# Performance work log

Hardware: AMD Instinct MI355X
Metric: run time of the kernel (lower is better)

Reference implementation:

```python
import math
import jax, jax.numpy as jnp
import numpy as np

L, H, K, NH, V, DFF = 6, 512, 512, 8, 64, 1024
B, T, S = 8, 512, 512
PAD = 0


def _ln(x, g, b, eps=1e-5):
    m = jnp.mean(x, -1, keepdims=True)
    v = jnp.mean((x - m) ** 2, -1, keepdims=True)
    return (x - m) * jax.lax.rsqrt(v + eps) * g + b


def _mha(Q, Kin, Vin, mask, wq, bq, wk, bk, wv, bv, wo, bo, g, b):
    # weights stored [in, out]
    B_, Tq, Hd = Q.shape
    dk = wq.shape[1] // NH
    dv = wv.shape[1] // NH
    q = (Q @ wq + bq).reshape(B_, Tq, NH, dk).transpose(0, 2, 1, 3)
    k = (Kin @ wk + bk).reshape(B_, -1, NH, dk).transpose(0, 2, 1, 3)
    v = (Vin @ wv + bv).reshape(B_, -1, NH, dv).transpose(0, 2, 1, 3)
    scores = jnp.einsum('bhqd,bhkd->bhqk', q, k) / jnp.sqrt(jnp.float32(dk))
    scores = jnp.where(mask[:, None, :, :], jnp.float32(-1e9), scores)
    attn = jax.nn.softmax(scores, axis=-1)
    ctx = jnp.einsum('bhqk,bhkd->bhqd', attn, v).transpose(0, 2, 1, 3).reshape(B_, Tq, Hd)
    return _ln(ctx @ wo + bo + Q, g, b)


def _pe(t, d):
    pos = jnp.arange(t, dtype=jnp.float32)[:, None]
    div = jnp.exp(jnp.arange(0, d, 2, dtype=jnp.float32) * (-math.log(10000.0) / d))
    pe = jnp.zeros((t, d), jnp.float32)
    pe = pe.at[:, 0::2].set(jnp.sin(pos * div)).at[:, 1::2].set(jnp.cos(pos * div))
    return pe


def setup_inputs() -> dict:
    key = jax.random.key(0)
    ks = iter(jax.random.split(key, 40))
    nrm = lambda shape, s=0.02: jax.random.normal(next(ks), shape, jnp.float32) * s
    inp = {
        'smiles_index': jax.random.randint(next(ks), (B, T), 0, V, dtype=jnp.int32),
        'enc_outputs': jax.random.normal(next(ks), (B, S, H), jnp.float32),
        'enc_pad_mask': jnp.zeros((B, 1, S), bool),
        'tgt_len': T,
        'mol_emb': nrm((V, H), 1.0).at[PAD].set(0.0),  # padding_idx=0 row zeroed
        # self-attn stacks [L, ...]
        'sa_wq': nrm((L, H, K)), 'sa_bq': jnp.zeros((L, K)),
        'sa_wk': nrm((L, H, K)), 'sa_bk': jnp.zeros((L, K)),
        'sa_wv': nrm((L, H, H)), 'sa_bv': jnp.zeros((L, H)),
        'sa_wo': nrm((L, H, H)), 'sa_bo': jnp.zeros((L, H)),
        'ln1_g': jnp.ones((L, H)), 'ln1_b': jnp.zeros((L, H)),
        # cross-attn stacks
        'ea_wq': nrm((L, H, K)), 'ea_bq': jnp.zeros((L, K)),
        'ea_wk': nrm((L, H, K)), 'ea_bk': jnp.zeros((L, K)),
        'ea_wv': nrm((L, H, H)), 'ea_bv': jnp.zeros((L, H)),
        'ea_wo': nrm((L, H, H)), 'ea_bo': jnp.zeros((L, H)),
        'ln2_g': jnp.ones((L, H)), 'ln2_b': jnp.zeros((L, H)),
        # conv1x1 FFN == per-position linear
        'c1_w': nrm((L, H, DFF)), 'c1_b': jnp.zeros((L, DFF)),
        'c2_w': nrm((L, DFF, H)), 'c2_b': jnp.zeros((L, H)),
        'ln3_g': jnp.ones((L, H)), 'ln3_b': jnp.zeros((L, H)),
    }
    return inp


def reference(smiles_index, enc_outputs, enc_pad_mask, tgt_len, mol_emb,
              sa_wq, sa_bq, sa_wk, sa_bk, sa_wv, sa_bv, sa_wo, sa_bo, ln1_g, ln1_b,
              ea_wq, ea_bq, ea_wk, ea_bk, ea_wv, ea_bv, ea_wo, ea_bo, ln2_g, ln2_b,
              c1_w, c1_b, c2_w, c2_b, ln3_g, ln3_b):
    b, t = smiles_index.shape
    s = enc_outputs.shape[1]
    # embeddings + sinusoidal positional encoding (dropout is identity in eval)
    x = mol_emb[smiles_index] + _pe(t, mol_emb.shape[1])[None]
    # masks: pad (key == pad_id) OR causal upper-triangular
    pad = (smiles_index == PAD)[:, None, :]                 # [B,1,T] -> broadcast over queries
    causal = jnp.triu(jnp.ones((t, t), bool), 1)[None]      # [1,T,T]
    self_mask = pad | causal                                # [B,T,T]
    enc_mask = jnp.broadcast_to(enc_pad_mask, (b, t, s))    # [B,T,S]
    for l in range(L):
        x = _mha(x, x, x, self_mask,
                 sa_wq[l], sa_bq[l], sa_wk[l], sa_bk[l], sa_wv[l], sa_bv[l],
                 sa_wo[l], sa_bo[l], ln1_g[l], ln1_b[l])
        x = _mha(x, enc_outputs, enc_outputs, enc_mask,
                 ea_wq[l], ea_bq[l], ea_wk[l], ea_bk[l], ea_wv[l], ea_bv[l],
                 ea_wo[l], ea_bo[l], ln2_g[l], ln2_b[l])
        h = jax.nn.relu(x @ c1_w[l] + c1_b[l])
        y = h @ c2_w[l] + c2_b[l]
        x = _ln(y + x, ln3_g[l], ln3_b[l])
    return x
```

## Files before the change

### kernel.cpp

```cpp
#include <hip/hip_runtime.h>
#include <hip/hip_bf16.h>
#include <math.h>

#define NL   6
#define HD   512
#define NHD  8
#define DK   64
#define DFFN 1024
#define NB   8
#define TT   512
#define MROWS (NB*TT)

typedef __hip_bfloat16 bf16;
typedef __attribute__((ext_vector_type(8))) short short8v;
typedef __attribute__((ext_vector_type(4))) float f32x4;

__device__ __forceinline__ float wave_sum(float v) {
#pragma unroll
  for (int off = 32; off; off >>= 1) v += __shfl_xor(v, off);
  return v;
}
__device__ __forceinline__ unsigned short f2bf(float x) {
  __hip_bfloat16 h = __float2bfloat16(x);
  return *reinterpret_cast<unsigned short*>(&h);
}

__device__ __forceinline__ void gload16(const void* g, void* l) {
  __builtin_amdgcn_global_load_lds(
      (const __attribute__((address_space(1))) unsigned int*)g,
      (__attribute__((address_space(3))) unsigned int*)l, 16, 0, 0);
}

__global__ __launch_bounds__(256)
void wprep_kernel(const float* __restrict__ W, bf16* __restrict__ Wt, int Kd, int Nd,
                  int dstRowOff, int dstSlabRows) {
  __shared__ float t[32][33];
  const size_t src = (size_t)blockIdx.z * Kd * Nd;
  const size_t dst = (size_t)blockIdx.z * dstSlabRows * Kd;
  const int n0 = blockIdx.x * 32, k0 = blockIdx.y * 32;
  const int tx = threadIdx.x & 31, ty = threadIdx.x >> 5;
#pragma unroll
  for (int j = 0; j < 4; ++j)
    t[ty + j * 8][tx] = W[src + (size_t)(k0 + ty + j * 8) * Nd + n0 + tx];
  __syncthreads();
#pragma unroll
  for (int j = 0; j < 4; ++j)
    Wt[dst + (size_t)(dstRowOff + n0 + ty + j * 8) * Kd + k0 + tx] =
        __float2bfloat16(t[tx][ty + j * 8]);
}

__global__ __launch_bounds__(256)
void bcat_kernel(const float* __restrict__ b0, const float* __restrict__ b1,
                 const float* __restrict__ b2, float* __restrict__ out, int nseg) {
  const int l = blockIdx.x;
  const int stride = 512 * nseg;
  for (int i = threadIdx.x; i < stride; i += 256) {
    const int seg = i >> 9, off = i & 511;
    const float* src = seg == 0 ? b0 : (seg == 1 ? b1 : b2);
    out[(size_t)l * stride + i] = src[(size_t)l * 512 + off];
  }
}

__global__ __launch_bounds__(256)
void cvtbf16_kernel(const float* __restrict__ in, unsigned short* __restrict__ out) {
  const int i = (blockIdx.x * 256 + threadIdx.x) * 4;
  float4 v = *(const float4*)(in + i);
  out[i + 0] = f2bf(v.x); out[i + 1] = f2bf(v.y);
  out[i + 2] = f2bf(v.z); out[i + 3] = f2bf(v.w);
}

__global__ __launch_bounds__(256)
void embed_pe_kernel(const int* __restrict__ idx, const float* __restrict__ emb,
                     float* __restrict__ x, unsigned short* __restrict__ xb) {
  const int row = blockIdx.x;
  const int t = row & (TT - 1);
  const int tok = idx[row];
  const float cdiv = -0.017988946009466842f;
#pragma unroll
  for (int e0 = 0; e0 < 2; ++e0) {
    const int e = threadIdx.x + e0 * 256;
    const float div = __expf((float)(e & ~1) * cdiv);
    const float ang = (float)t * div;
    const float pe = (e & 1) ? cosf(ang) : sinf(ang);
    const float v = emb[(size_t)tok * HD + e] + pe;
    x[(size_t)row * HD + e] = v;
    xb[(size_t)row * HD + e] = f2bf(v);
  }
}

template<int TN, int OUT_BF16, int RELU>
__global__ __launch_bounds__(256)
void mgemm2_kernel(const bf16* __restrict__ A, const bf16* __restrict__ Bt,
                   const float* __restrict__ bias, float* __restrict__ Cf,
                   unsigned short* __restrict__ Cb, int M, int N, int K) {
  constexpr int NR = TN / 32;
  constexpr int BJ = TN / 32;
  __shared__ __attribute__((aligned(16))) char As[2][128 * 128];
  __shared__ __attribute__((aligned(16))) char Bs[2][TN * 128];

  const int tid = threadIdx.x, w = tid >> 6, lane = tid & 63;
  const int wm = w >> 1, wn = w & 1;
  const int m0 = blockIdx.x * 128, n0 = blockIdx.y * TN;
  const int lrow = lane >> 3;
  const int lchk = (lane & 7) ^ lrow;

  const bf16* ga[4];
#pragma unroll
  for (int j = 0; j < 4; ++j)
    ga[j] = A + (size_t)(m0 + w * 32 + j * 8 + lrow) * K + lchk * 8;
  const bf16* gb[BJ];
#pragma unroll
  for (int j = 0; j < BJ; ++j)
    gb[j] = Bt + (size_t)(n0 + w * (8 * BJ) + j * 8 + lrow) * K + lchk * 8;

  f32x4 acc[4][NR];
#pragma unroll
  for (int fm = 0; fm < 4; ++fm)
#pragma unroll
    for (int fn = 0; fn < NR; ++fn) acc[fm][fn] = (f32x4){0.f, 0.f, 0.f, 0.f};

  const int l4 = lane & 15;
  const int khb = (lane >> 4) * 16;

  auto issue = [&](int t, int buf) {
#pragma unroll
    for (int j = 0; j < 4; ++j)
      gload16(ga[j] + t * 64, &As[buf][(w * 32 + j * 8) * 128]);
#pragma unroll
    for (int j = 0; j < BJ; ++j)
      gload16(gb[j] + t * 64, &Bs[buf][(w * (8 * BJ) + j * 8) * 128]);
  };
  auto compute = [&](int buf) {
#pragma unroll
    for (int kk = 0; kk < 2; ++kk) {
      short8v af[4], bfv[NR];
#pragma unroll
      for (int fm = 0; fm < 4; ++fm) {
        const int r = wm * 64 + fm * 16 + l4;
        af[fm] = *(const short8v*)(&As[buf][r * 128 + ((kk * 64 + khb) ^ ((r & 7) << 4))]);
      }
#pragma unroll
      for (int fn = 0; fn < NR; ++fn) {
        const int r = wn * (TN / 2) + fn * 16 + l4;
        bfv[fn] = *(const short8v*)(&Bs[buf][r * 128 + ((kk * 64 + khb) ^ ((r & 7) << 4))]);
      }
#pragma unroll
      for (int fm = 0; fm < 4; ++fm)
#pragma unroll
        for (int fn = 0; fn < NR; ++fn)
          acc[fm][fn] = __builtin_amdgcn_mfma_f32_16x16x32_bf16(af[fm], bfv[fn], acc[fm][fn], 0, 0, 0);
    }
  };

  const int NT = K >> 6;
  issue(0, 0);
  for (int t = 0; t < NT; ++t) {
    __syncthreads();
    if (t + 1 < NT) issue(t + 1, (t + 1) & 1);
    compute(t & 1);
  }

  const int crow = (lane >> 4) * 4, ccol = l4;
#pragma unroll
  for (int fm = 0; fm < 4; ++fm)
#pragma unroll
    for (int fn = 0; fn < NR; ++fn) {
      const int gr = m0 + wm * 64 + fm * 16 + crow;
      const int gc = n0 + wn * (TN / 2) + fn * 16 + ccol;
      const float bs = bias[gc];
#pragma unroll
      for (int r = 0; r < 4; ++r) {
        float vv = acc[fm][fn][r] + bs;
        if (RELU) vv = fmaxf(vv, 0.f);
        if (OUT_BF16) Cb[(size_t)(gr + r) * N + gc] = f2bf(vv);
        else          Cf[(size_t)(gr + r) * N + gc] = vv;
      }
    }
}

template<int CAUSAL>
__global__ __launch_bounds__(256)
void mattn_kernel(const unsigned short* __restrict__ q, const unsigned short* __restrict__ kgl,
                  const unsigned short* __restrict__ vgl, unsigned short* __restrict__ ctx,
                  const int* __restrict__ idx, const unsigned char* __restrict__ emask,
                  int qstride, int kvstride) {
  __shared__ __attribute__((aligned(16))) unsigned short kt[64 * 64];
  __shared__ __attribute__((aligned(16))) unsigned short vt[64 * 64];
  __shared__ __attribute__((aligned(16))) unsigned short pl[4][16 * 64];
  __shared__ float km[64];

  const int bh = blockIdx.x;
  const int b = bh >> 3, h = bh & 7;
  const int qbase = blockIdx.y * 64;
  const int tid = threadIdx.x, w = tid >> 6, lane = tid & 63;
  const int l4 = lane & 15, g = lane >> 4;

  const unsigned short* qp = q + (size_t)(b * TT + qbase + w * 16 + l4) * qstride + h * DK + g * 8;
  short8v aq0 = *(const short8v*)qp;
  short8v aq1 = *(const short8v*)(qp + 32);

  float m_r[4], l_r[4];
  f32x4 acc_o[4];
#pragma unroll
  for (int r = 0; r < 4; ++r) { m_r[r] = -1e30f; l_r[r] = 0.f; }
#pragma unroll
  for (int f = 0; f < 4; ++f) acc_o[f] = (f32x4){0.f, 0.f, 0.f, 0.f};

  const int kvEnd = CAUSAL ? (qbase + 64) : TT;
  for (int kt0 = 0; kt0 < kvEnd; kt0 += 64) {
    __syncthreads();
    if (tid < 64) {
      const int kp = b * TT + kt0 + tid;
      const bool mk = CAUSAL ? (idx[kp] == 0) : (emask[kp] != 0);
      km[tid] = mk ? 1.f : 0.f;
    }
    {
      const int r = tid >> 2;
      const int bc = (tid & 3) * 32;
      const unsigned short* kp = kgl + (size_t)(b * TT + kt0 + r) * kvstride + h * DK + (bc >> 1);
      short8v ka = *(const short8v*)kp;
      short8v kb2 = *(const short8v*)(kp + 8);
      const int sw = (r & 7) << 4;
      *(short8v*)((char*)kt + r * 128 + (bc ^ sw)) = ka;
      *(short8v*)((char*)kt + r * 128 + ((bc + 16) ^ sw)) = kb2;
    }
    {
      const int k2 = (tid & 31) * 2;
      const int d0 = (tid >> 5) * 8;
      const unsigned short* vp0 = vgl + (size_t)(b * TT + kt0 + k2) * kvstride + h * DK + d0;
      const unsigned short* vp1 = vp0 + kvstride;
      short8v v0 = *(const short8v*)vp0;
      short8v v1 = *(const short8v*)vp1;
#pragma unroll
      for (int j = 0; j < 8; ++j) {
        const int d = d0 + j;
        const unsigned pk = ((unsigned)(unsigned short)v0[j]) | (((unsigned)(unsigned short)v1[j]) << 16);
        *(unsigned*)((char*)vt + d * 128 + ((k2 * 2) ^ ((d & 7) << 4))) = pk;
      }
    }
    __syncthreads();

    f32x4 s4[4];
#pragma unroll
    for (int f = 0; f < 4; ++f) {
      const int krow = f * 16 + l4;
      const int sw = (krow & 7) << 4;
      short8v bk0 = *(const short8v*)((const char*)kt + krow * 128 + ((g * 16) ^ sw));
      short8v bk1 = *(const short8v*)((const char*)kt + krow * 128 + ((64 + g * 16) ^ sw));
      f32x4 a = {};
      a = __builtin_amdgcn_mfma_f32_16x16x32_bf16(aq0, bk0, a, 0, 0, 0);
      a = __builtin_amdgcn_mfma_f32_16x16x32_bf16(aq1, bk1, a, 0, 0, 0);
      s4[f] = a;
    }

    float sc_r[4];
#pragma unroll
    for (int r = 0; r < 4; ++r) {
      const int qpos = qbase + w * 16 + g * 4 + r;
      float sf[4];
#pragma unroll
      for (int f = 0; f < 4; ++f) {
        const int kpos = kt0 + f * 16 + l4;
        float s = s4[f][r] * 0.125f;
        const bool msk = (km[f * 16 + l4] != 0.f) || (CAUSAL && kpos > qpos);
        sf[f] = msk ? -1e9f : s;
      }
      float mx = fmaxf(fmaxf(sf[0], sf[1]), fmaxf(sf[2], sf[3]));
#pragma unroll
      for (int off = 8; off; off >>= 1) mx = fmaxf(mx, __shfl_xor(mx, off));
      const float mn = fmaxf(m_r[r], mx);
      const float sc = __expf(m_r[r] - mn);
      m_r[r] = mn;
      sc_r[r] = sc;
      float ps = 0.f;
      const int prow = g * 4 + r;
      const int psw = (prow & 7) << 4;
#pragma unroll
      for (int f = 0; f < 4; ++f) {
        const float p = __expf(sf[f] - mn);
        ps += p;
        *(unsigned short*)((char*)pl[w] + prow * 128 + ((f * 32 + l4 * 2) ^ psw)) = f2bf(p);
      }
#pragma unroll
      for (int off = 8; off; off >>= 1) ps += __shfl_xor(ps, off);
      l_r[r] = l_r[r] * sc + ps;
    }

#pragma unroll
    for (int f = 0; f < 4; ++f)
#pragma unroll
      for (int r = 0; r < 4; ++r) acc_o[f][r] *= sc_r[r];

    const int asw = (l4 & 7) << 4;
    short8v pa0 = *(const short8v*)((const char*)pl[w] + l4 * 128 + ((g * 16) ^ asw));
    short8v pa1 = *(const short8v*)((const char*)pl[w] + l4 * 128 + ((g * 16 + 64) ^ asw));
#pragma unroll
    for (int f = 0; f < 4; ++f) {
      const int drow = f * 16 + l4;
      const int sw = (drow & 7) << 4;
      short8v vb0 = *(const short8v*)((const char*)vt + drow * 128 + ((g * 16) ^ sw));
      short8v vb1 = *(const short8v*)((const char*)vt + drow * 128 + ((g * 16 + 64) ^ sw));
      acc_o[f] = __builtin_amdgcn_mfma_f32_16x16x32_bf16(pa0, vb0, acc_o[f], 0, 0, 0);
      acc_o[f] = __builtin_amdgcn_mfma_f32_16x16x32_bf16(pa1, vb1, acc_o[f], 0, 0, 0);
    }
  }

  float rl[4];
#pragma unroll
  for (int r = 0; r < 4; ++r) rl[r] = 1.f / l_r[r];
#pragma unroll
  for (int f = 0; f < 4; ++f)
#pragma unroll
    for (int r = 0; r < 4; ++r) {
      const int row = qbase + w * 16 + g * 4 + r;
      const int col = h * DK + f * 16 + l4;
      ctx[(size_t)(b * TT + row) * HD + col] = f2bf(acc_o[f][r] * rl[r]);
    }
}

__global__ __launch_bounds__(256)
void ln_kernel(const float* __restrict__ y, const float* __restrict__ res,
               float* __restrict__ out, unsigned short* __restrict__ outb,
               const float* __restrict__ g, const float* __restrict__ bta) {
  const int row = blockIdx.x;
  const int tid = threadIdx.x;
  const int w = tid >> 6, lane = tid & 63;
  const float* yr = y + (size_t)row * HD;
  const float* rr = res + (size_t)row * HD;

  float v0 = yr[tid] + rr[tid];
  float v1 = yr[tid + 256] + rr[tid + 256];

  __shared__ float red[4];
  float s = wave_sum(v0 + v1);
  if (lane == 0) red[w] = s;
  __syncthreads();
  const float mean = (red[0] + red[1] + red[2] + red[3]) * (1.f / HD);
  __syncthreads();

  const float d0 = v0 - mean, d1 = v1 - mean;
  float qv = wave_sum(d0 * d0 + d1 * d1);
  if (lane == 0) red[w] = qv;
  __syncthreads();
  const float var = (red[0] + red[1] + red[2] + red[3]) * (1.f / HD);
  const float rstd = rsqrtf(var + 1e-5f);

  const float o0 = d0 * rstd * g[tid] + bta[tid];
  const float o1 = d1 * rstd * g[tid + 256] + bta[tid + 256];
  out[(size_t)row * HD + tid] = o0;
  out[(size_t)row * HD + tid + 256] = o1;
  outb[(size_t)row * HD + tid] = f2bf(o0);
  outb[(size_t)row * HD + tid + 256] = f2bf(o1);
}

extern "C" void kernel_launch(void* const* d_in, const int* in_sizes, int n_in,
                              void* d_out, int out_size, void* d_ws, size_t ws_size,
                              hipStream_t stream) {
  const int* idx = (const int*)d_in[0];
  const float* enc = (const float*)d_in[1];
  const unsigned char* emask = (const unsigned char*)d_in[2];
  const float* emb = (const float*)d_in[4];
  const float* sa_wq = (const float*)d_in[5];
  const float* sa_bq = (const float*)d_in[6];
  const float* sa_wk = (const float*)d_in[7];
  const float* sa_bk = (const float*)d_in[8];
  const float* sa_wv = (const float*)d_in[9];
  const float* sa_bv = (const float*)d_in[10];
  const float* sa_wo = (const float*)d_in[11];
  const float* sa_bo = (const float*)d_in[12];
  const float* ln1g = (const float*)d_in[13];
  const float* ln1b = (const float*)d_in[14];
  const float* ea_wq = (const float*)d_in[15];
  const float* ea_bq = (const float*)d_in[16];
  const float* ea_wk = (const float*)d_in[17];
  const float* ea_bk = (const float*)d_in[18];
  const float* ea_wv = (const float*)d_in[19];
  const float* ea_bv = (const float*)d_in[20];
  const float* ea_wo = (const float*)d_in[21];
  const float* ea_bo = (const float*)d_in[22];
  const float* ln2g = (const float*)d_in[23];
  const float* ln2b = (const float*)d_in[24];
  const float* c1w = (const float*)d_in[25];
  const float* c1b = (const float*)d_in[26];
  const float* c2w = (const float*)d_in[27];
  const float* c2b = (const float*)d_in[28];
  const float* ln3g = (const float*)d_in[29];
  const float* ln3b = (const float*)d_in[30];

  const size_t MH = (size_t)MROWS * HD;
  const size_t SQ = (size_t)HD * HD;
  char* ws = (char*)d_ws;
  float*          x    = (float*)(ws + 0);
  unsigned short* xb   = (unsigned short*)(ws + (8u << 20));
  unsigned short* qkvb = (unsigned short*)(ws + (12u << 20));
  unsigned short* qcb  = (unsigned short*)(ws + (24u << 20));
  unsigned short* kvb  = (unsigned short*)(ws + (28u << 20));
  unsigned short* cxb  = (unsigned short*)(ws + (36u << 20));
  float*          yb   = (float*)(ws + (40u << 20));
  unsigned short* encb = (unsigned short*)(ws + (48u << 20));
  bf16*           wt   = (bf16*)(ws + (52u << 20));
  float*          bcS  = (float*)(ws + (92u << 20));
  float*          bcKV = (float*)(ws + (93u << 20));
  unsigned short* hb   = qkvb;

  bf16* t_saqkv = wt;
  bf16* t_sao   = wt + 18 * SQ;
  bf16* t_eaq   = wt + 24 * SQ;
  bf16* t_eakv  = wt + 30 * SQ;
  bf16* t_eao   = wt + 42 * SQ;
  bf16* t_c1    = wt + 48 * SQ;
  bf16* t_c2    = wt + 60 * SQ;

  const dim3 blk(256);
  const dim3 gQKV(MROWS / 128, 1536 / 128);
  const dim3 g1024(MROWS / 128, 1024 / 128);
  const dim3 g512n(MROWS / 128, 512 / 64);
  const dim3 attng(NB * NHD, TT / 64);

  wprep_kernel<<<dim3(16, 16, NL), blk, 0, stream>>>(sa_wq, t_saqkv, HD, HD, 0, 1536);
  wprep_kernel<<<dim3(16, 16, NL), blk, 0, stream>>>(sa_wk, t_saqkv, HD, HD, 512, 1536);
  wprep_kernel<<<dim3(16, 16, NL), blk, 0, stream>>>(sa_wv, t_saqkv, HD, HD, 1024, 1536);
  wprep_kernel<<<dim3(16, 16, NL), blk, 0, stream>>>(sa_wo, t_sao, HD, HD, 0, 512);
  wprep_kernel<<<dim3(16, 16, NL), blk, 0, stream>>>(ea_wq, t_eaq, HD, HD, 0, 512);
  wprep_kernel<<<dim3(16, 16, NL), blk, 0, stream>>>(ea_wk, t_eakv, HD, HD, 0, 1024);
  wprep_kernel<<<dim3(16, 16, NL), blk, 0, stream>>>(ea_wv, t_eakv, HD, HD, 512, 1024);
  wprep_kernel<<<dim3(16, 16, NL), blk, 0, stream>>>(ea_wo, t_eao, HD, HD, 0, 512);
  wprep_kernel<<<dim3(32, 16, NL), blk, 0, stream>>>(c1w, t_c1, HD, DFFN, 0, 1024);
  wprep_kernel<<<dim3(16, 32, NL), blk, 0, stream>>>(c2w, t_c2, DFFN, HD, 0, 512);
  bcat_kernel<<<NL, blk, 0, stream>>>(sa_bq, sa_bk, sa_bv, bcS, 3);
  bcat_kernel<<<NL, blk, 0, stream>>>(ea_bk, ea_bv, nullptr, bcKV, 2);
  cvtbf16_kernel<<<MH / 1024, blk, 0, stream>>>(enc, encb);

  embed_pe_kernel<<<MROWS, blk, 0, stream>>>(idx, emb, x, xb);

  for (int l = 0; l < NL; ++l) {
    const size_t b512 = (size_t)l * HD;
    const size_t bFF = (size_t)l * DFFN;

    mgemm2_kernel<128, 1, 0><<<gQKV, blk, 0, stream>>>(
        (const bf16*)xb, t_saqkv + (size_t)l * 3 * SQ, bcS + (size_t)l * 1536,
        nullptr, qkvb, MROWS, 1536, HD);
    mattn_kernel<1><<<attng, blk, 0, stream>>>(qkvb, qkvb + 512, qkvb + 1024, cxb,
                                               idx, emask, 1536, 1536);
    mgemm2_kernel<64, 0, 0><<<g512n, blk, 0, stream>>>(
        (const bf16*)cxb, t_sao + (size_t)l * SQ, sa_bo + b512, yb, nullptr, MROWS, HD, HD);
    ln_kernel<<<MROWS, blk, 0, stream>>>(yb, x, x, xb, ln1g + b512, ln1b + b512);

    mgemm2_kernel<64, 1, 0><<<g512n, blk, 0, stream>>>(
        (const bf16*)xb, t_eaq + (size_t)l * SQ, ea_bq + b512, nullptr, qcb, MROWS, HD, HD);
    mgemm2_kernel<128, 1, 0><<<g1024, blk, 0, stream>>>(
        (const bf16*)encb, t_eakv + (size_t)l * 2 * SQ, bcKV + (size_t)l * 1024,
        nullptr, kvb, MROWS, 1024, HD);
    mattn_kernel<0><<<attng, blk, 0, stream>>>(qcb, kvb, kvb + 512, cxb,
                                               idx, emask, 512, 1024);
    mgemm2_kernel<64, 0, 0><<<g512n, blk, 0, stream>>>(
        (const bf16*)cxb, t_eao + (size_t)l * SQ, ea_bo + b512, yb, nullptr, MROWS, HD, HD);
    ln_kernel<<<MROWS, blk, 0, stream>>>(yb, x, x, xb, ln2g + b512, ln2b + b512);

    mgemm2_kernel<128, 1, 1><<<g1024, blk, 0, stream>>>(
        (const bf16*)xb, t_c1 + (size_t)l * 2 * SQ, c1b + bFF, nullptr, hb, MROWS, DFFN, HD);
    mgemm2_kernel<64, 0, 0><<<g512n, blk, 0, stream>>>(
        (const bf16*)hb, t_c2 + (size_t)l * 2 * SQ, c2b + b512, yb, nullptr, MROWS, HD, DFFN);
    ln_kernel<<<MROWS, blk, 0, stream>>>(yb, x, x, xb, ln3g + b512, ln3b + b512);
  }

  hipMemcpyAsync(d_out, x, MH * sizeof(float), hipMemcpyDeviceToDevice, stream);
}
```

Baseline: 941.8 us.

## Retile GEMMs to 64x128 with split-K, enlarge attention blocks, skip masked causal tiles

The GEMM kernel is retiled to 64x128 blocks of two waves, and the N=512 projections (output projections and FFN down) use a 2-way split-K. The two fp32 partial sums are added inside a new layernorm kernel, so no separate reduction pass is needed. Attention blocks grow to 512 threads covering 128 queries, fully masked causal tiles are skipped per wave, the causal compare runs only on diagonal tiles, and the pad mask becomes an additive bias. MFMA sections are wrapped in s_setprio. The aim is more blocks in flight and less wasted causal work, at the cost of extra fp32 partial-sum traffic and larger attention blocks.

```diff
diff --git a/kernel.cpp b/kernel.cpp
--- a/kernel.cpp
+++ b/kernel.cpp
@@ -13,6 +13,7 @@
 
 typedef __hip_bfloat16 bf16;
 typedef __attribute__((ext_vector_type(8))) short short8v;
+typedef __attribute__((ext_vector_type(4))) short short4v;
 typedef __attribute__((ext_vector_type(4))) float f32x4;
 
 __device__ __forceinline__ float wave_sum(float v) {
@@ -88,71 +89,71 @@
   }
 }
 
-template<int TN, int OUT_BF16, int RELU>
-__global__ __launch_bounds__(256)
-void mgemm2_kernel(const bf16* __restrict__ A, const bf16* __restrict__ Bt,
+template<int SPLITK, int OUT_BF16, int RELU>
+__global__ __launch_bounds__(128)
+void mgemm3_kernel(const bf16* __restrict__ A, const bf16* __restrict__ Bt,
                    const float* __restrict__ bias, float* __restrict__ Cf,
                    unsigned short* __restrict__ Cb, int M, int N, int K) {
-  constexpr int NR = TN / 32;
-  constexpr int BJ = TN / 32;
-  __shared__ __attribute__((aligned(16))) char As[2][128 * 128];
-  __shared__ __attribute__((aligned(16))) char Bs[2][TN * 128];
+  __shared__ __attribute__((aligned(16))) char As[2][64 * 128];
+  __shared__ __attribute__((aligned(16))) char Bs[2][128 * 128];
 
   const int tid = threadIdx.x, w = tid >> 6, lane = tid & 63;
-  const int wm = w >> 1, wn = w & 1;
-  const int m0 = blockIdx.x * 128, n0 = blockIdx.y * TN;
+  const int m0 = blockIdx.x * 64, n0 = blockIdx.y * 128;
+  const int Ksl = K / SPLITK;
+  const int kb = blockIdx.z * Ksl;
   const int lrow = lane >> 3;
   const int lchk = (lane & 7) ^ lrow;
 
   const bf16* ga[4];
 #pragma unroll
   for (int j = 0; j < 4; ++j)
-    ga[j] = A + (size_t)(m0 + w * 32 + j * 8 + lrow) * K + lchk * 8;
-  const bf16* gb[BJ];
-#pragma unroll
-  for (int j = 0; j < BJ; ++j)
-    gb[j] = Bt + (size_t)(n0 + w * (8 * BJ) + j * 8 + lrow) * K + lchk * 8;
-
-  f32x4 acc[4][NR];
+    ga[j] = A + (size_t)(m0 + w * 32 + j * 8 + lrow) * K + kb + lchk * 8;
+  const bf16* gb[8];
+#pragma unroll
+  for (int j = 0; j < 8; ++j)
+    gb[j] = Bt + (size_t)(n0 + w * 64 + j * 8 + lrow) * K + kb + lchk * 8;
+
+  f32x4 acc[4][4];
 #pragma unroll
   for (int fm = 0; fm < 4; ++fm)
 #pragma unroll
-    for (int fn = 0; fn < NR; ++fn) acc[fm][fn] = (f32x4){0.f, 0.f, 0.f, 0.f};
-
-  const int l4 = lane & 15;
-  const int khb = (lane >> 4) * 16;
+    for (int fn = 0; fn < 4; ++fn) acc[fm][fn] = (f32x4){0.f, 0.f, 0.f, 0.f};
+
+  const int l4 = lane & 15, khb = (lane >> 4) * 16;
 
   auto issue = [&](int t, int buf) {
 #pragma unroll
     for (int j = 0; j < 4; ++j)
       gload16(ga[j] + t * 64, &As[buf][(w * 32 + j * 8) * 128]);
 #pragma unroll
-    for (int j = 0; j < BJ; ++j)
-      gload16(gb[j] + t * 64, &Bs[buf][(w * (8 * BJ) + j * 8) * 128]);
+    for (int j = 0; j < 8; ++j)
+      gload16(gb[j] + t * 64, &Bs[buf][(w * 64 + j * 8) * 128]);
   };
   auto compute = [&](int buf) {
 #pragma unroll
     for (int kk = 0; kk < 2; ++kk) {
-      short8v af[4], bfv[NR];
+      short8v af[4], bfv[4];
 #pragma unroll
       for (int fm = 0; fm < 4; ++fm) {
-        const int r = wm * 64 + fm * 16 + l4;
+        const int r = fm * 16 + l4;
         af[fm] = *(const short8v*)(&As[buf][r * 128 + ((kk * 64 + khb) ^ ((r & 7) << 4))]);
       }
 #pragma unroll
-      for (int fn = 0; fn < NR; ++fn) {
-        const int r = wn * (TN / 2) + fn * 16 + l4;
+      for (int fn = 0; fn < 4; ++fn) {
+        const int r = w * 64 + fn * 16 + l4;
         bfv[fn] = *(const short8v*)(&Bs[buf][r * 128 + ((kk * 64 + khb) ^ ((r & 7) << 4))]);
       }
+      __builtin_amdgcn_s_setprio(1);
 #pragma unroll
       for (int fm = 0; fm < 4; ++fm)
 #pragma unroll
-        for (int fn = 0; fn < NR; ++fn)
+        for (int fn = 0; fn < 4; ++fn)
           acc[fm][fn] = __builtin_amdgcn_mfma_f32_16x16x32_bf16(af[fm], bfv[fn], acc[fm][fn], 0, 0, 0);
+      __builtin_amdgcn_s_setprio(0);
     }
   };
 
-  const int NT = K >> 6;
+  const int NT = Ksl >> 6;
   issue(0, 0);
   for (int t = 0; t < NT; ++t) {
     __syncthreads();
@@ -164,34 +165,34 @@
 #pragma unroll
   for (int fm = 0; fm < 4; ++fm)
 #pragma unroll
-    for (int fn = 0; fn < NR; ++fn) {
-      const int gr = m0 + wm * 64 + fm * 16 + crow;
-      const int gc = n0 + wn * (TN / 2) + fn * 16 + ccol;
-      const float bs = bias[gc];
+    for (int fn = 0; fn < 4; ++fn) {
+      const int gr = m0 + fm * 16 + crow;
+      const int gc = n0 + w * 64 + fn * 16 + ccol;
+      const float bs = ((SPLITK == 1 || blockIdx.z == 0) && bias) ? bias[gc] : 0.f;
 #pragma unroll
       for (int r = 0; r < 4; ++r) {
         float vv = acc[fm][fn][r] + bs;
         if (RELU) vv = fmaxf(vv, 0.f);
         if (OUT_BF16) Cb[(size_t)(gr + r) * N + gc] = f2bf(vv);
-        else          Cf[(size_t)(gr + r) * N + gc] = vv;
+        else Cf[(size_t)blockIdx.z * M * N + (size_t)(gr + r) * N + gc] = vv;
       }
     }
 }
 
 template<int CAUSAL>
-__global__ __launch_bounds__(256)
+__global__ __launch_bounds__(512)
 void mattn_kernel(const unsigned short* __restrict__ q, const unsigned short* __restrict__ kgl,
                   const unsigned short* __restrict__ vgl, unsigned short* __restrict__ ctx,
                   const int* __restrict__ idx, const unsigned char* __restrict__ emask,
                   int qstride, int kvstride) {
   __shared__ __attribute__((aligned(16))) unsigned short kt[64 * 64];
   __shared__ __attribute__((aligned(16))) unsigned short vt[64 * 64];
-  __shared__ __attribute__((aligned(16))) unsigned short pl[4][16 * 64];
+  __shared__ __attribute__((aligned(16))) unsigned short pl[8][16 * 64];
   __shared__ float km[64];
 
   const int bh = blockIdx.x;
   const int b = bh >> 3, h = bh & 7;
-  const int qbase = blockIdx.y * 64;
+  const int qbase = blockIdx.y * 128;
   const int tid = threadIdx.x, w = tid >> 6, lane = tid & 63;
   const int l4 = lane & 15, g = lane >> 4;
 
@@ -206,102 +207,112 @@
 #pragma unroll
   for (int f = 0; f < 4; ++f) acc_o[f] = (f32x4){0.f, 0.f, 0.f, 0.f};
 
-  const int kvEnd = CAUSAL ? (qbase + 64) : TT;
+  const int kvEnd = CAUSAL ? (qbase + 128) : TT;
   for (int kt0 = 0; kt0 < kvEnd; kt0 += 64) {
     __syncthreads();
     if (tid < 64) {
       const int kp = b * TT + kt0 + tid;
       const bool mk = CAUSAL ? (idx[kp] == 0) : (emask[kp] != 0);
-      km[tid] = mk ? 1.f : 0.f;
+      km[tid] = mk ? -1e9f : 0.f;
     }
     {
-      const int r = tid >> 2;
-      const int bc = (tid & 3) * 32;
-      const unsigned short* kp = kgl + (size_t)(b * TT + kt0 + r) * kvstride + h * DK + (bc >> 1);
-      short8v ka = *(const short8v*)kp;
-      short8v kb2 = *(const short8v*)(kp + 8);
-      const int sw = (r & 7) << 4;
-      *(short8v*)((char*)kt + r * 128 + (bc ^ sw)) = ka;
-      *(short8v*)((char*)kt + r * 128 + ((bc + 16) ^ sw)) = kb2;
+      const int r = tid >> 3, c8 = tid & 7;
+      const unsigned short* kp = kgl + (size_t)(b * TT + kt0 + r) * kvstride + h * DK + c8 * 8;
+      short8v kv = *(const short8v*)kp;
+      *(short8v*)((char*)kt + r * 128 + ((c8 * 16) ^ ((r & 7) << 4))) = kv;
     }
     {
       const int k2 = (tid & 31) * 2;
-      const int d0 = (tid >> 5) * 8;
-      const unsigned short* vp0 = vgl + (size_t)(b * TT + kt0 + k2) * kvstride + h * DK + d0;
+      const int d4 = (tid >> 5) * 4;
+      const unsigned short* vp0 = vgl + (size_t)(b * TT + kt0 + k2) * kvstride + h * DK + d4;
       const unsigned short* vp1 = vp0 + kvstride;
-      short8v v0 = *(const short8v*)vp0;
-      short8v v1 = *(const short8v*)vp1;
-#pragma unroll
-      for (int j = 0; j < 8; ++j) {
-        const int d = d0 + j;
+      short4v v0 = *(const short4v*)vp0;
+      short4v v1 = *(const short4v*)vp1;
+#pragma unroll
+      for (int j = 0; j < 4; ++j) {
+        const int d = d4 + j;
         const unsigned pk = ((unsigned)(unsigned short)v0[j]) | (((unsigned)(unsigned short)v1[j]) << 16);
         *(unsigned*)((char*)vt + d * 128 + ((k2 * 2) ^ ((d & 7) << 4))) = pk;
       }
     }
     __syncthreads();
 
-    f32x4 s4[4];
-#pragma unroll
-    for (int f = 0; f < 4; ++f) {
-      const int krow = f * 16 + l4;
-      const int sw = (krow & 7) << 4;
-      short8v bk0 = *(const short8v*)((const char*)kt + krow * 128 + ((g * 16) ^ sw));
-      short8v bk1 = *(const short8v*)((const char*)kt + krow * 128 + ((64 + g * 16) ^ sw));
-      f32x4 a = {};
-      a = __builtin_amdgcn_mfma_f32_16x16x32_bf16(aq0, bk0, a, 0, 0, 0);
-      a = __builtin_amdgcn_mfma_f32_16x16x32_bf16(aq1, bk1, a, 0, 0, 0);
-      s4[f] = a;
-    }
-
-    float sc_r[4];
-#pragma unroll
-    for (int r = 0; r < 4; ++r) {
-      const int qpos = qbase + w * 16 + g * 4 + r;
-      float sf[4];
+    if (!(CAUSAL && kt0 > qbase + w * 16 + 15)) {
+      const bool diag = CAUSAL && (kt0 + 64 > qbase + w * 16);
+
+      f32x4 s4[4];
+      __builtin_amdgcn_s_setprio(1);
 #pragma unroll
       for (int f = 0; f < 4; ++f) {
-        const int kpos = kt0 + f * 16 + l4;
-        float s = s4[f][r] * 0.125f;
-        const bool msk = (km[f * 16 + l4] != 0.f) || (CAUSAL && kpos > qpos);
-        sf[f] = msk ? -1e9f : s;
-      }
-      float mx = fmaxf(fmaxf(sf[0], sf[1]), fmaxf(sf[2], sf[3]));
-#pragma unroll
-      for (int off = 8; off; off >>= 1) mx = fmaxf(mx, __shfl_xor(mx, off));
-      const float mn = fmaxf(m_r[r], mx);
-      const float sc = __expf(m_r[r] - mn);
-      m_r[r] = mn;
-      sc_r[r] = sc;
-      float ps = 0.f;
-      const int prow = g * 4 + r;
-      const int psw = (prow & 7) << 4;
+        const int krow = f * 16 + l4;
+        const int sw = (krow & 7) << 4;
+        short8v bk0 = *(const short8v*)((const char*)kt + krow * 128 + ((g * 16) ^ sw));
+        short8v bk1 = *(const short8v*)((const char*)kt + krow * 128 + ((64 + g * 16) ^ sw));
+        f32x4 a = {};
+        a = __builtin_amdgcn_mfma_f32_16x16x32_bf16(aq0, bk0, a, 0, 0, 0);
+        a = __builtin_amdgcn_mfma_f32_16x16x32_bf16(aq1, bk1, a, 0, 0, 0);
+        s4[f] = a;
+      }
+      __builtin_amdgcn_s_setprio(0);
+
+      float kmb[4];
+#pragma unroll
+      for (int f = 0; f < 4; ++f) kmb[f] = km[f * 16 + l4];
+
+      float sc_r[4];
+#pragma unroll
+      for (int r = 0; r < 4; ++r) {
+        const int qpos = qbase + w * 16 + g * 4 + r;
+        float sf[4];
+#pragma unroll
+        for (int f = 0; f < 4; ++f) sf[f] = fmaf(s4[f][r], 0.125f, kmb[f]);
+        if (diag) {
+#pragma unroll
+          for (int f = 0; f < 4; ++f) {
+            const int kpos = kt0 + f * 16 + l4;
+            sf[f] = (kpos > qpos) ? -1e9f : sf[f];
+          }
+        }
+        float mx = fmaxf(fmaxf(sf[0], sf[1]), fmaxf(sf[2], sf[3]));
+#pragma unroll
+        for (int off = 8; off; off >>= 1) mx = fmaxf(mx, __shfl_xor(mx, off));
+        const float mn = fmaxf(m_r[r], mx);
+        const float sc = __expf(m_r[r] - mn);
+        m_r[r] = mn;
+        sc_r[r] = sc;
+        float ps = 0.f;
+        const int prow = g * 4 + r;
+        const int psw = (prow & 7) << 4;
+#pragma unroll
+        for (int f = 0; f < 4; ++f) {
+          const float p = __expf(sf[f] - mn);
+          ps += p;
+          *(unsigned short*)((char*)pl[w] + prow * 128 + ((f * 32 + l4 * 2) ^ psw)) = f2bf(p);
+        }
+#pragma unroll
+        for (int off = 8; off; off >>= 1) ps += __shfl_xor(ps, off);
+        l_r[r] = l_r[r] * sc + ps;
+      }
+
+#pragma unroll
+      for (int f = 0; f < 4; ++f)
+#pragma unroll
+        for (int r = 0; r < 4; ++r) acc_o[f][r] *= sc_r[r];
+
+      const int asw = (l4 & 7) << 4;
+      short8v pa0 = *(const short8v*)((const char*)pl[w] + l4 * 128 + ((g * 16) ^ asw));
+      short8v pa1 = *(const short8v*)((const char*)pl[w] + l4 * 128 + ((g * 16 + 64) ^ asw));
+      __builtin_amdgcn_s_setprio(1);
 #pragma unroll
       for (int f = 0; f < 4; ++f) {
-        const float p = __expf(sf[f] - mn);
-        ps += p;
-        *(unsigned short*)((char*)pl[w] + prow * 128 + ((f * 32 + l4 * 2) ^ psw)) = f2bf(p);
-      }
-#pragma unroll
-      for (int off = 8; off; off >>= 1) ps += __shfl_xor(ps, off);
-      l_r[r] = l_r[r] * sc + ps;
-    }
-
-#pragma unroll
-    for (int f = 0; f < 4; ++f)
-#pragma unroll
-      for (int r = 0; r < 4; ++r) acc_o[f][r] *= sc_r[r];
-
-    const int asw = (l4 & 7) << 4;
-    short8v pa0 = *(const short8v*)((const char*)pl[w] + l4 * 128 + ((g * 16) ^ asw));
-    short8v pa1 = *(const short8v*)((const char*)pl[w] + l4 * 128 + ((g * 16 + 64) ^ asw));
-#pragma unroll
-    for (int f = 0; f < 4; ++f) {
-      const int drow = f * 16 + l4;
-      const int sw = (drow & 7) << 4;
-      short8v vb0 = *(const short8v*)((const char*)vt + drow * 128 + ((g * 16) ^ sw));
-      short8v vb1 = *(const short8v*)((const char*)vt + drow * 128 + ((g * 16 + 64) ^ sw));
-      acc_o[f] = __builtin_amdgcn_mfma_f32_16x16x32_bf16(pa0, vb0, acc_o[f], 0, 0, 0);
-      acc_o[f] = __builtin_amdgcn_mfma_f32_16x16x32_bf16(pa1, vb1, acc_o[f], 0, 0, 0);
+        const int drow = f * 16 + l4;
+        const int sw = (drow & 7) << 4;
+        short8v vb0 = *(const short8v*)((const char*)vt + drow * 128 + ((g * 16) ^ sw));
+        short8v vb1 = *(const short8v*)((const char*)vt + drow * 128 + ((g * 16 + 64) ^ sw));
+        acc_o[f] = __builtin_amdgcn_mfma_f32_16x16x32_bf16(pa0, vb0, acc_o[f], 0, 0, 0);
+        acc_o[f] = __builtin_amdgcn_mfma_f32_16x16x32_bf16(pa1, vb1, acc_o[f], 0, 0, 0);
+      }
+      __builtin_amdgcn_s_setprio(0);
     }
   }
 
@@ -319,17 +330,17 @@
 }
 
 __global__ __launch_bounds__(256)
-void ln_kernel(const float* __restrict__ y, const float* __restrict__ res,
-               float* __restrict__ out, unsigned short* __restrict__ outb,
-               const float* __restrict__ g, const float* __restrict__ bta) {
+void ln3_kernel(const float* __restrict__ y0, const float* __restrict__ y1,
+                const float* __restrict__ res, float* __restrict__ out,
+                unsigned short* __restrict__ outb,
+                const float* __restrict__ g, const float* __restrict__ bta) {
   const int row = blockIdx.x;
   const int tid = threadIdx.x;
   const int w = tid >> 6, lane = tid & 63;
-  const float* yr = y + (size_t)row * HD;
-  const float* rr = res + (size_t)row * HD;
-
-  float v0 = yr[tid] + rr[tid];
-  float v1 = yr[tid + 256] + rr[tid + 256];
+  const size_t ro = (size_t)row * HD;
+
+  float v0 = y0[ro + tid] + y1[ro + tid] + res[ro + tid];
+  float v1 = y0[ro + tid + 256] + y1[ro + tid + 256] + res[ro + tid + 256];
 
   __shared__ float red[4];
   float s = wave_sum(v0 + v1);
@@ -347,10 +358,10 @@
 
   const float o0 = d0 * rstd * g[tid] + bta[tid];
   const float o1 = d1 * rstd * g[tid + 256] + bta[tid + 256];
-  out[(size_t)row * HD + tid] = o0;
-  out[(size_t)row * HD + tid + 256] = o1;
-  outb[(size_t)row * HD + tid] = f2bf(o0);
-  outb[(size_t)row * HD + tid + 256] = f2bf(o1);
+  out[ro + tid] = o0;
+  out[ro + tid + 256] = o1;
+  outb[ro + tid] = f2bf(o0);
+  outb[ro + tid + 256] = f2bf(o1);
 }
 
 extern "C" void kernel_launch(void* const* d_in, const int* in_sizes, int n_in,
@@ -396,11 +407,11 @@
   unsigned short* qcb  = (unsigned short*)(ws + (24u << 20));
   unsigned short* kvb  = (unsigned short*)(ws + (28u << 20));
   unsigned short* cxb  = (unsigned short*)(ws + (36u << 20));
-  float*          yb   = (float*)(ws + (40u << 20));
-  unsigned short* encb = (unsigned short*)(ws + (48u << 20));
-  bf16*           wt   = (bf16*)(ws + (52u << 20));
-  float*          bcS  = (float*)(ws + (92u << 20));
-  float*          bcKV = (float*)(ws + (93u << 20));
+  float*          y0   = (float*)(ws + (40u << 20));
+  unsigned short* encb = (unsigned short*)(ws + (56u << 20));
+  bf16*           wt   = (bf16*)(ws + (60u << 20));
+  float*          bcS  = (float*)(ws + (98u << 20));
+  float*          bcKV = (float*)(ws + (99u << 20));
   unsigned short* hb   = qkvb;
 
   bf16* t_saqkv = wt;
@@ -412,10 +423,14 @@
   bf16* t_c2    = wt + 60 * SQ;
 
   const dim3 blk(256);
-  const dim3 gQKV(MROWS / 128, 1536 / 128);
-  const dim3 g1024(MROWS / 128, 1024 / 128);
-  const dim3 g512n(MROWS / 128, 512 / 64);
-  const dim3 attng(NB * NHD, TT / 64);
+  const dim3 blk128(128);
+  const dim3 blk512(512);
+  const dim3 gQKV(MROWS / 64, 1536 / 128);
+  const dim3 g1024(MROWS / 64, 1024 / 128);
+  const dim3 g512u(MROWS / 64, 512 / 128);
+  const dim3 g512s(MROWS / 64, 512 / 128, 2);
+  const dim3 gFF2s(MROWS / 64, 512 / 128, 2);
+  const dim3 attng(NB * NHD, TT / 128);
 
   wprep_kernel<<<dim3(16, 16, NL), blk, 0, stream>>>(sa_wq, t_saqkv, HD, HD, 0, 1536);
   wprep_kernel<<<dim3(16, 16, NL), blk, 0, stream>>>(sa_wk, t_saqkv, HD, HD, 512, 1536);
@@ -437,31 +452,31 @@
     const size_t b512 = (size_t)l * HD;
     const size_t bFF = (size_t)l * DFFN;
 
-    mgemm2_kernel<128, 1, 0><<<gQKV, blk, 0, stream>>>(
+    mgemm3_kernel<1, 1, 0><<<gQKV, blk128, 0, stream>>>(
         (const bf16*)xb, t_saqkv + (size_t)l * 3 * SQ, bcS + (size_t)l * 1536,
         nullptr, qkvb, MROWS, 1536, HD);
-    mattn_kernel<1><<<attng, blk, 0, stream>>>(qkvb, qkvb + 512, qkvb + 1024, cxb,
-                                               idx, emask, 1536, 1536);
-    mgemm2_kernel<64, 0, 0><<<g512n, blk, 0, stream>>>(
-        (const bf16*)cxb, t_sao + (size_t)l * SQ, sa_bo + b512, yb, nullptr, MROWS, HD, HD);
-    ln_kernel<<<MROWS, blk, 0, stream>>>(yb, x, x, xb, ln1g + b512, ln1b + b512);
-
-    mgemm2_kernel<64, 1, 0><<<g512n, blk, 0, stream>>>(
+    mattn_kernel<1><<<attng, blk512, 0, stream>>>(qkvb, qkvb + 512, qkvb + 1024, cxb,
+                                                  idx, emask, 1536, 1536);
+    mgemm3_kernel<2, 0, 0><<<g512s, blk128, 0, stream>>>(
+        (const bf16*)cxb, t_sao + (size_t)l * SQ, sa_bo + b512, y0, nullptr, MROWS, HD, HD);
+    ln3_kernel<<<MROWS, blk, 0, stream>>>(y0, y0 + MH, x, x, xb, ln1g + b512, ln1b + b512);
+
+    mgemm3_kernel<1, 1, 0><<<g512u, blk128, 0, stream>>>(
         (const bf16*)xb, t_eaq + (size_t)l * SQ, ea_bq + b512, nullptr, qcb, MROWS, HD, HD);
-    mgemm2_kernel<128, 1, 0><<<g1024, blk, 0, stream>>>(
+    mgemm3_kernel<1, 1, 0><<<g1024, blk128, 0, stream>>>(
         (const bf16*)encb, t_eakv + (size_t)l * 2 * SQ, bcKV + (size_t)l * 1024,
         nullptr, kvb, MROWS, 1024, HD);
-    mattn_kernel<0><<<attng, blk, 0, stream>>>(qcb, kvb, kvb + 512, cxb,
-                                               idx, emask, 512, 1024);
-    mgemm2_kernel<64, 0, 0><<<g512n, blk, 0, stream>>>(
-        (const bf16*)cxb, t_eao + (size_t)l * SQ, ea_bo + b512, yb, nullptr, MROWS, HD, HD);
-    ln_kernel<<<MROWS, blk, 0, stream>>>(yb, x, x, xb, ln2g + b512, ln2b + b512);
-
-    mgemm2_kernel<128, 1, 1><<<g1024, blk, 0, stream>>>(
+    mattn_kernel<0><<<attng, blk512, 0, stream>>>(qcb, kvb, kvb + 512, cxb,
+                                                  idx, emask, 512, 1024);
+    mgemm3_kernel<2, 0, 0><<<g512s, blk128, 0, stream>>>(
+        (const bf16*)cxb, t_eao + (size_t)l * SQ, ea_bo + b512, y0, nullptr, MROWS, HD, HD);
+    ln3_kernel<<<MROWS, blk, 0, stream>>>(y0, y0 + MH, x, x, xb, ln2g + b512, ln2b + b512);
+
+    mgemm3_kernel<1, 1, 1><<<g1024, blk128, 0, stream>>>(
         (const bf16*)xb, t_c1 + (size_t)l * 2 * SQ, c1b + bFF, nullptr, hb, MROWS, DFFN, HD);
-    mgemm2_kernel<64, 0, 0><<<g512n, blk, 0, stream>>>(
-        (const bf16*)hb, t_c2 + (size_t)l * 2 * SQ, c2b + b512, yb, nullptr, MROWS, HD, DFFN);
-    ln_kernel<<<MROWS, blk, 0, stream>>>(yb, x, x, xb, ln3g + b512, ln3b + b512);
+    mgemm3_kernel<2, 0, 0><<<gFF2s, blk128, 0, stream>>>(
+        (const bf16*)hb, t_c2 + (size_t)l * 2 * SQ, c2b + b512, y0, nullptr, MROWS, HD, DFFN);
+    ln3_kernel<<<MROWS, blk, 0, stream>>>(y0, y0 + MH, x, x, xb, ln3g + b512, ln3b + b512);
   }
 
   hipMemcpyAsync(d_out, x, MH * sizeof(float), hipMemcpyDeviceToDevice, stream);
```

Result: slower. 1.014 ms (+7.7%).
